# Performance work log

Hardware: AMD Instinct MI355X
Metric: run time of the kernel (lower is better)

Reference implementation:

```python
import jax, jax.numpy as jnp
import numpy as np

_N, _S, _D, _E0 = 30000, 16, 64, 100000


def _build_topology():
    """Windowed subgraphs: root i owns nodes i..i+S-1. Local random edges."""
    N, S, E0 = _N, _S, _E0
    R = N - S + 1                      # number of roots
    rng = np.random.default_rng(0)
    rootid = np.repeat(np.arange(R), S).astype(np.int32)          # [M] tuple -> root i
    nodeid = (rootid + np.tile(np.arange(S), R)).astype(np.int32)  # [M] tuple -> node j
    diag_tuple = (np.arange(R, dtype=np.int64) * S).astype(np.int32)  # tuple index of (i,i)
    # local edges u -> v = u+delta, 1 <= delta < S, so some subgraphs contain both endpoints
    u = rng.integers(0, N - S, E0)
    delta = rng.integers(1, S, E0)
    v = u + delta
    # roots i whose subgraph contains both u and v: max(v-S+1,0) <= i <= u
    lo = np.maximum(v - S + 1, 0)
    cnt = u - lo + 1
    total = int(cnt.sum())
    base = np.repeat(np.cumsum(cnt) - cnt, cnt)
    roots = np.repeat(lo, cnt) + (np.arange(total) - base)
    u_r = np.repeat(u, cnt)
    v_r = np.repeat(v, cnt)
    t_u = roots * S + (u_r - roots)    # tuple index of (i,u)
    t_v = roots * S + (v_r - roots)    # tuple index of (i,v)
    # undirected edge -> both message directions at tuple level
    msg_tgt = np.concatenate([t_u, t_v]).astype(np.int32)
    msg_src = np.concatenate([t_v, t_u]).astype(np.int32)
    return rootid, nodeid, diag_tuple, msg_tgt, msg_src, R


def setup_inputs() -> dict:
    rootid, nodeid, diag_tuple, msg_tgt, msg_src, R = _build_topology()
    M, D = R * _S, _D
    key = jax.random.key(0)
    kx, k0, k1 = jax.random.split(key, 3)
    X = jax.random.normal(kx, (M, D), jnp.float32)
    W0 = jax.random.normal(k0, (D, D), jnp.float32) / np.sqrt(D)
    b0 = jnp.zeros((D,), jnp.float32)
    W1 = jax.random.normal(k1, (3 * D, D), jnp.float32) / np.sqrt(3 * D)
    b1 = jnp.zeros((D,), jnp.float32)
    return {
        "X": X, "W0": W0, "b0": b0, "W1": W1, "b1": b1,
        "rootid": jnp.asarray(rootid), "nodeid": jnp.asarray(nodeid),
        "diag_tuple": jnp.asarray(diag_tuple),
        "msg_tgt": jnp.asarray(msg_tgt), "msg_src": jnp.asarray(msg_src),
        "N": _N,
    }


def reference(X, W0, b0, W1, b1, rootid, nodeid, diag_tuple, msg_tgt, msg_src, N):
    M = X.shape[0]
    R = diag_tuple.shape[0]
    # lin0 (MLP numlayer=1, tailact): tuplewise Linear + ReLU
    H = jax.nn.relu(X @ W0 + b0)                                    # [M, D]
    # 2D message passing on subgraphs: X'_{ij} = sum_{k in N(j)} H_{ik}
    Xmp = jax.ops.segment_sum(H[msg_src], msg_tgt, num_segments=M)  # [M, D]
    ones = jnp.ones((M, 1), X.dtype)
    # diag X_{ii} -> broadcast over subgraph (unpool4subg)
    X1 = Xmp[diag_tuple][rootid]                                    # [M, D]
    # pool over subgraph members j (mean), broadcast back per root i
    Psum = jax.ops.segment_sum(Xmp, rootid, num_segments=R)
    Pcnt = jax.ops.segment_sum(ones, rootid, num_segments=R)
    X2 = (Psum / jnp.maximum(Pcnt, 1.0))[rootid]                    # [M, D]
    # cross-subgraph pool over roots i per node j (mean), broadcast back per node j
    Qsum = jax.ops.segment_sum(Xmp, nodeid, num_segments=N)
    Qcnt = jax.ops.segment_sum(ones, nodeid, num_segments=N)
    X3 = (Qsum / jnp.maximum(Qcnt, 1.0))[nodeid]                    # [M, D]
    # catvalue order: [X2, X1, X3], then final MLP (single Linear)
    return jnp.concatenate([X2, X1, X3], axis=-1) @ W1 + b1         # [M, outdim]
```

## Files before the change

kernel.cpp:

```cpp
#include <hip/hip_runtime.h>

#define S 16
#define D 64
#define G 16
#define PROWS 31
#define PSTR 66
#define PREG 2048
#define XSTR 136
#define ZSTR 68

typedef __attribute__((ext_vector_type(8))) short bf16x8;
typedef __attribute__((ext_vector_type(4))) float f32x4;

union BF8 { unsigned u[4]; bf16x8 v; };

__device__ __forceinline__ unsigned pk2bf(float x, float y) {
    unsigned ux = __float_as_uint(x) + 0x8000u;
    unsigned uy = __float_as_uint(y) + 0x8000u;
    return __builtin_amdgcn_perm(uy, ux, 0x07060302);
}
__device__ __forceinline__ bf16x8 pk8(float a, float b, float c, float d,
                                      float e, float f, float g, float h) {
    BF8 t;
    t.u[0] = pk2bf(a, b); t.u[1] = pk2bf(c, d);
    t.u[2] = pk2bf(e, f); t.u[3] = pk2bf(g, h);
    return t.v;
}
__device__ __forceinline__ unsigned short f2bf_rhu(float x) {
    return (unsigned short)((__float_as_uint(x) + 0x8000u) >> 16);
}
__device__ __forceinline__ short f2bf(float f) {
    unsigned u = __float_as_uint(f);
    u += 0x7fffu + ((u >> 16) & 1u);
    return (short)(u >> 16);
}

__global__ void k_counts(const int* __restrict__ msg_tgt, const int* __restrict__ msg_src,
                         unsigned long long* __restrict__ Q, int E2,
                         const float* __restrict__ W0, const float* __restrict__ W1,
                         unsigned short* __restrict__ W0T, unsigned short* __restrict__ WabT,
                         unsigned short* __restrict__ WcT) {
    int idx = blockIdx.x * 256 + threadIdx.x;
    if (idx < 4096) {
        int d = idx >> 6, k = idx & 63;
        W0T[d * 64 + k] = (unsigned short)f2bf(W0[k * 64 + d]);
    } else if (idx < 12288) {
        int o = idx - 4096; int d = o >> 7, e = o & 127;
        WabT[d * 128 + e] = (unsigned short)f2bf(W1[e * 64 + d]);
    } else if (idx < 16384) {
        int o = idx - 12288; int d = o >> 6, e = o & 63;
        WcT[d * 64 + e] = (unsigned short)f2bf(W1[(128 + e) * 64 + d]);
    }
    if (idx >= E2) return;
    int t = msg_tgt[idx];
    if (t & 15) return;
    int delta = msg_src[idx] & 15;
    int u = t >> 4;
    atomicAdd(&Q[2 * u + 1], 1ull << (4 * delta));
    atomicAdd(&Q[2 * (u + delta)], 1ull << (64 - 4 * delta));
}

__global__ __launch_bounds__(256, 4) void k_root(
    const float* __restrict__ X, const float* __restrict__ b0,
    const unsigned short* __restrict__ W0T,
    const unsigned long long* __restrict__ Q,
    const unsigned short* __restrict__ WabT, const float* __restrict__ b1,
    float* __restrict__ Y, float* __restrict__ Qpart, int R)
{
    __shared__ float part[4 * PREG];
    __shared__ unsigned short x2x1[G][XSTR];
    int grp = blockIdx.x;
    int tid = threadIdx.x, lane = tid & 63, w = tid >> 6, m = lane & 15, q = lane >> 4;
    const ulonglong2* Q2 = (const ulonglong2*)Q;

    {
        float4 z = {0.f, 0.f, 0.f, 0.f};
#pragma unroll
        for (int i = 0; i < 8; i++)
            *(float4*)&part[w * PREG + i * 256 + lane * 4] = z;
    }

    bf16x8 bB[8];
    float bv[4];
#pragma unroll
    for (int cg = 0; cg < 4; cg++) {
        const bf16x8* wr = (const bf16x8*)(W0T + (size_t)(cg * 16 + m) * 64);
        bB[cg * 2] = wr[q]; bB[cg * 2 + 1] = wr[4 + q];
        bv[cg] = b0[cg * 16 + m];
    }

    int bp0 = (((2 * q) * 16 + m) & 63) * 4;
    int bp1 = (((2 * q + 1) * 16 + m) & 63) * 4;

    int root0 = grp * G;
    int gmax = R - root0; if (gmax > G) gmax = G;
    const float* Xg = X + (size_t)root0 * S * D;

    float4 xa, xb, xc, xd; ulonglong2 qq;
    if (w < gmax) {
        const float* xr = Xg + ((size_t)w * S + m) * D + q * 8;
        xa = *(const float4*)(xr);
        xb = *(const float4*)(xr + 4);
        xc = *(const float4*)(xr + 32);
        xd = *(const float4*)(xr + 36);
        qq = Q2[(size_t)(root0 + w) + m];
    }

    for (int g = w; g < gmax; g += 4) {
        float4 nxa, nxb, nxc, nxd; ulonglong2 nqq;
        int gn = g + 4;
        bool pf = (gn < gmax);
        if (pf) {
            const float* xr = Xg + ((size_t)gn * S + m) * D + q * 8;
            nxa = *(const float4*)(xr);
            nxb = *(const float4*)(xr + 4);
            nxc = *(const float4*)(xr + 32);
            nxd = *(const float4*)(xr + 36);
            nqq = Q2[(size_t)(root0 + gn) + m];
        }

        bf16x8 a0 = pk8(xa.x, xa.y, xa.z, xa.w, xb.x, xb.y, xb.z, xb.w);
        bf16x8 a1 = pk8(xc.x, xc.y, xc.z, xc.w, xd.x, xd.y, xd.z, xd.w);
        unsigned hp0[4], hp1[4];
#pragma unroll
        for (int cg = 0; cg < 4; cg++) {
            f32x4 c = {bv[cg], bv[cg], bv[cg], bv[cg]};
            c = __builtin_amdgcn_mfma_f32_16x16x32_bf16(a0, bB[cg * 2], c, 0, 0, 0);
            c = __builtin_amdgcn_mfma_f32_16x16x32_bf16(a1, bB[cg * 2 + 1], c, 0, 0, 0);
            hp0[cg] = pk2bf(fmaxf(c[0], 0.f), fmaxf(c[1], 0.f));
            hp1[cg] = pk2bf(fmaxf(c[2], 0.f), fmaxf(c[3], 0.f));
        }

        unsigned long long cw = (qq.y << (4 * m)) | ((qq.x >> (63 - 4 * m)) >> 1);
        unsigned w32 = (q == 0) ? (unsigned)cw : ((q == 1) ? (unsigned)(cw >> 32) : 0u);
        bf16x8 A2 = pk8((float)((w32 >> 0) & 15u),  (float)((w32 >> 4) & 15u),
                        (float)((w32 >> 8) & 15u),  (float)((w32 >> 12) & 15u),
                        (float)((w32 >> 16) & 15u), (float)((w32 >> 20) & 15u),
                        (float)((w32 >> 24) & 15u), (float)((w32 >> 28) & 15u));

        BF8 b2[4];
#pragma unroll
        for (int cg = 0; cg < 4; cg++) {
            b2[cg].u[0] = __builtin_amdgcn_ds_bpermute(bp0, (int)hp0[cg]);
            b2[cg].u[1] = __builtin_amdgcn_ds_bpermute(bp0, (int)hp1[cg]);
            b2[cg].u[2] = __builtin_amdgcn_ds_bpermute(bp1, (int)hp0[cg]);
            b2[cg].u[3] = __builtin_amdgcn_ds_bpermute(bp1, (int)hp1[cg]);
        }

        f32x4 xm[4];
#pragma unroll
        for (int cg = 0; cg < 4; cg++) {
            f32x4 z4 = {0.f, 0.f, 0.f, 0.f};
            xm[cg] = __builtin_amdgcn_mfma_f32_16x16x32_bf16(A2, b2[cg].v, z4, 0, 0, 0);
        }

        float ps[4], x1[4];
#pragma unroll
        for (int cg = 0; cg < 4; cg++)
            ps[cg] = (xm[cg][0] + xm[cg][1]) + (xm[cg][2] + xm[cg][3]);
#pragma unroll
        for (int cg = 0; cg < 4; cg++) ps[cg] += __shfl_xor(ps[cg], 16);
#pragma unroll
        for (int cg = 0; cg < 4; cg++) ps[cg] += __shfl_xor(ps[cg], 32);
#pragma unroll
        for (int cg = 0; cg < 4; cg++) x1[cg] = __shfl(xm[cg][0], m);
        if (q == 0) {
#pragma unroll
            for (int cg = 0; cg < 4; cg++) {
                x2x1[g][cg * 16 + m]      = f2bf_rhu(ps[cg] * (1.f / 16.f));
                x2x1[g][64 + cg * 16 + m] = f2bf_rhu(x1[cg]);
            }
        }

        int rb = g + q * 4;
#pragma unroll
        for (int cg = 0; cg < 4; cg++) {
            float* pw = &part[w * PREG + rb * PSTR + cg * 16 + m];
            pw[0 * PSTR] += xm[cg][0];
            pw[1 * PSTR] += xm[cg][1];
            pw[2 * PSTR] += xm[cg][2];
            pw[3 * PSTR] += xm[cg][3];
        }

        if (pf) { xa = nxa; xb = nxb; xc = nxc; xd = nxd; qq = nqq; }
    }
    __syncthreads();

    {
        float bvy = b1[w * 16 + m];
        f32x4 c = {bvy, bvy, bvy, bvy};
        const bf16x8* brow = (const bf16x8*)(WabT + (size_t)(w * 16 + m) * 128);
#pragma unroll
        for (int kh = 0; kh < 4; kh++) {
            bf16x8 a = *(const bf16x8*)&x2x1[m][kh * 32 + q * 8];
            c = __builtin_amdgcn_mfma_f32_16x16x32_bf16(a, brow[kh * 4 + q], c, 0, 0, 0);
        }
#pragma unroll
        for (int r = 0; r < 4; r++) {
            int row = root0 + q * 4 + r;
            if (row < R) Y[(size_t)row * 64 + w * 16 + m] = c[r];
        }
    }

    float* qp = Qpart + (size_t)grp * (PROWS * 64);
    for (int idx = tid; idx < PROWS * 32; idx += 256) {
        int r = idx >> 5, c2 = (idx & 31) * 2;
        int o = r * PSTR + c2;
        float2 s0 = *(float2*)&part[o];
        float2 s1 = *(float2*)&part[PREG + o];
        float2 s2 = *(float2*)&part[2 * PREG + o];
        float2 s3 = *(float2*)&part[3 * PREG + o];
        float2 v;
        v.x = s0.x + s1.x + s2.x + s3.x;
        v.y = s0.y + s1.y + s2.y + s3.y;
        *(float2*)&qp[r * 64 + c2] = v;
    }
}

__global__ __launch_bounds__(256) void k_linzout(
    const float* __restrict__ Qpart, const unsigned short* __restrict__ WcT,
    const float* __restrict__ Y, float4* __restrict__ out, int R, int N)
{
    __shared__ float zb[16 * ZSTR];
    int tid = threadIdx.x, lane = tid & 63, w = tid >> 6, m = lane & 15, q = lane >> 4;
    int row0 = blockIdx.x * 16;
    int n = row0 + m;
    float inv = 0.f;
    int gLo = 0, gHi = -1;
    if (n < N) {
        int lo = n - (S - 1); if (lo < 0) lo = 0;
        int hi = (n < R - 1) ? n : (R - 1);
        inv = 1.f / (float)(hi - lo + 1);
        gLo = lo >> 4; gHi = hi >> 4;
    }
    f32x4 c = {0.f, 0.f, 0.f, 0.f};
    const bf16x8* brow = (const bf16x8*)(WcT + (size_t)(w * 16 + m) * 64);
#pragma unroll
    for (int kh = 0; kh < 2; kh++) {
        int k0 = kh * 32 + q * 8;
        float4 u = {0.f, 0.f, 0.f, 0.f}, v = {0.f, 0.f, 0.f, 0.f};
        for (int g = gLo; g <= gHi; g++) {
            const float* src = Qpart + ((size_t)g * PROWS + (n - g * 16)) * 64 + k0;
            float4 uu = *(const float4*)src, vv = *(const float4*)(src + 4);
            u.x += uu.x; u.y += uu.y; u.z += uu.z; u.w += uu.w;
            v.x += vv.x; v.y += vv.y; v.z += vv.z; v.w += vv.w;
        }
        bf16x8 a = pk8(u.x * inv, u.y * inv, u.z * inv, u.w * inv,
                       v.x * inv, v.y * inv, v.z * inv, v.w * inv);
        c = __builtin_amdgcn_mfma_f32_16x16x32_bf16(a, brow[kh * 4 + q], c, 0, 0, 0);
    }
#pragma unroll
    for (int r = 0; r < 4; r++)
        zb[(q * 4 + r) * ZSTR + w * 16 + m] = c[r];
    __syncthreads();

    const float4* Y4 = (const float4*)Y;
#pragma unroll 4
    for (int it = 0; it < 16; ++it) {
        int nl = it;
        int nn = row0 + nl;
        if (nn >= N) break;
        int d4 = tid & 15, ii = tid >> 4;
        int lo = nn - (S - 1); if (lo < 0) lo = 0;
        int hi = (nn < R - 1) ? nn : (R - 1);
        int i = lo + ii;
        if (i > hi) continue;
        int t = i * 16 + (nn - i);
        float4 yv = Y4[(size_t)i * 16 + d4];
        float4 zv = *(float4*)&zb[nl * ZSTR + d4 * 4];
        float4 o;
        o.x = yv.x + zv.x; o.y = yv.y + zv.y; o.z = yv.z + zv.z; o.w = yv.w + zv.w;
        out[(size_t)t * 16 + d4] = o;
    }
}

extern "C" void kernel_launch(void* const* d_in, const int* in_sizes, int n_in,
                              void* d_out, int out_size, void* d_ws, size_t ws_size,
                              hipStream_t stream) {
    (void)n_in; (void)out_size; (void)ws_size;
    const float* X  = (const float*)d_in[0];
    const float* W0 = (const float*)d_in[1];
    const float* b0 = (const float*)d_in[2];
    const float* W1 = (const float*)d_in[3];
    const float* b1 = (const float*)d_in[4];
    const int* msg_tgt = (const int*)d_in[8];
    const int* msg_src = (const int*)d_in[9];
    const int M = in_sizes[5];
    const int R = in_sizes[7];
    const int E = in_sizes[8];
    const int N = R + S - 1;

    char* p = (char*)d_ws;
    unsigned long long* Q = (unsigned long long*)p; p += (size_t)N * 16;
    float* Y    = (float*)p;             p += (size_t)R * 64 * 4;
    unsigned short* W0T  = (unsigned short*)p; p += (size_t)4096 * 2;
    unsigned short* WabT = (unsigned short*)p; p += (size_t)8192 * 2;
    unsigned short* WcT  = (unsigned short*)p; p += (size_t)4096 * 2;

    int NG = (R + G - 1) / G;
    float* Qpart = (float*)d_out;

    hipMemsetAsync(Q, 0, (size_t)N * 16, stream);
    int E2 = E >> 1;
    int CB = (E2 > 16384 ? E2 : 16384);
    k_counts<<<(CB + 255) / 256, 256, 0, stream>>>(msg_tgt, msg_src, Q, E2,
                                                   W0, W1, W0T, WabT, WcT);
    k_root<<<NG, 256, 0, stream>>>(X, b0, W0T, Q, WabT, b1, Y, Qpart, R);
    int NB = (N + 15) / 16;
    k_linzout<<<NB, 256, 0, stream>>>(Qpart, WcT, Y, (float4*)d_out, R, N);
    (void)M;
}
```

Baseline: 275.7 us.

## Compute transposed message MFMA for vectorized partial-sum accumulation and interleave X2/X1

Adds a second MFMA with swapped operands so each lane holds four consecutive columns of the message result. The per-wave shared-memory partial sums can then be read and written as float4 instead of scalar read-modify-writes, with the row stride padded to 68 for alignment. X2 and X1 are packed together into one 32-bit store per column, and the W1 rows are permuted at conversion time to match the interleaved order. The untransposed MFMA result supplies X1 directly, which removes a shuffle. The cost is four extra MFMAs per group and a larger shared-memory footprint.

```diff
diff --git a/kernel.cpp b/kernel.cpp
--- a/kernel.cpp
+++ b/kernel.cpp
@@ -4,8 +4,8 @@
 #define D 64
 #define G 16
 #define PROWS 31
-#define PSTR 66
-#define PREG 2048
+#define PSTR 68
+#define PREG 2176
 #define XSTR 136
 #define ZSTR 68
 
@@ -25,9 +25,6 @@
     t.u[0] = pk2bf(a, b); t.u[1] = pk2bf(c, d);
     t.u[2] = pk2bf(e, f); t.u[3] = pk2bf(g, h);
     return t.v;
-}
-__device__ __forceinline__ unsigned short f2bf_rhu(float x) {
-    return (unsigned short)((__float_as_uint(x) + 0x8000u) >> 16);
 }
 __device__ __forceinline__ short f2bf(float f) {
     unsigned u = __float_as_uint(f);
@@ -46,7 +43,8 @@
         W0T[d * 64 + k] = (unsigned short)f2bf(W0[k * 64 + d]);
     } else if (idx < 12288) {
         int o = idx - 4096; int d = o >> 7, e = o & 127;
-        WabT[d * 128 + e] = (unsigned short)f2bf(W1[e * 64 + d]);
+        int knew = (e < 64) ? (2 * e) : (2 * (e - 64) + 1);
+        WabT[d * 128 + knew] = (unsigned short)f2bf(W1[e * 64 + d]);
     } else if (idx < 16384) {
         int o = idx - 12288; int d = o >> 6, e = o & 63;
         WcT[d * 64 + e] = (unsigned short)f2bf(W1[(128 + e) * 64 + d]);
@@ -78,6 +76,8 @@
 #pragma unroll
         for (int i = 0; i < 8; i++)
             *(float4*)&part[w * PREG + i * 256 + lane * 4] = z;
+        float2 z2 = {0.f, 0.f};
+        *(float2*)&part[w * PREG + 2048 + lane * 2] = z2;
     }
 
     bf16x8 bB[8];
@@ -107,6 +107,11 @@
     }
 
     for (int g = w; g < gmax; g += 4) {
+        float* pbase = &part[w * PREG + (g + m) * PSTR + 4 * q];
+        float4 pr[4];
+#pragma unroll
+        for (int cg = 0; cg < 4; cg++) pr[cg] = *(float4*)&pbase[cg * 16];
+
         float4 nxa, nxb, nxc, nxd; ulonglong2 nqq;
         int gn = g + 4;
         bool pf = (gn < gmax);
@@ -147,39 +152,37 @@
             b2[cg].u[3] = __builtin_amdgcn_ds_bpermute(bp1, (int)hp1[cg]);
         }
 
-        f32x4 xm[4];
+        f32x4 xmt[4];
 #pragma unroll
         for (int cg = 0; cg < 4; cg++) {
             f32x4 z4 = {0.f, 0.f, 0.f, 0.f};
-            xm[cg] = __builtin_amdgcn_mfma_f32_16x16x32_bf16(A2, b2[cg].v, z4, 0, 0, 0);
+            xmt[cg] = __builtin_amdgcn_mfma_f32_16x16x32_bf16(b2[cg].v, A2, z4, 0, 0, 0);
         }
 
         float ps[4], x1[4];
 #pragma unroll
-        for (int cg = 0; cg < 4; cg++)
-            ps[cg] = (xm[cg][0] + xm[cg][1]) + (xm[cg][2] + xm[cg][3]);
+        for (int cg = 0; cg < 4; cg++) {
+            f32x4 z4 = {0.f, 0.f, 0.f, 0.f};
+            f32x4 xu = __builtin_amdgcn_mfma_f32_16x16x32_bf16(A2, b2[cg].v, z4, 0, 0, 0);
+            ps[cg] = (xu[0] + xu[1]) + (xu[2] + xu[3]);
+            x1[cg] = xu[0];
+        }
 #pragma unroll
         for (int cg = 0; cg < 4; cg++) ps[cg] += __shfl_xor(ps[cg], 16);
 #pragma unroll
         for (int cg = 0; cg < 4; cg++) ps[cg] += __shfl_xor(ps[cg], 32);
-#pragma unroll
-        for (int cg = 0; cg < 4; cg++) x1[cg] = __shfl(xm[cg][0], m);
         if (q == 0) {
 #pragma unroll
-            for (int cg = 0; cg < 4; cg++) {
-                x2x1[g][cg * 16 + m]      = f2bf_rhu(ps[cg] * (1.f / 16.f));
-                x2x1[g][64 + cg * 16 + m] = f2bf_rhu(x1[cg]);
-            }
-        }
-
-        int rb = g + q * 4;
-#pragma unroll
-        for (int cg = 0; cg < 4; cg++) {
-            float* pw = &part[w * PREG + rb * PSTR + cg * 16 + m];
-            pw[0 * PSTR] += xm[cg][0];
-            pw[1 * PSTR] += xm[cg][1];
-            pw[2 * PSTR] += xm[cg][2];
-            pw[3 * PSTR] += xm[cg][3];
+            for (int cg = 0; cg < 4; cg++)
+                *(unsigned*)&x2x1[g][2 * (cg * 16 + m)] =
+                    pk2bf(ps[cg] * (1.f / 16.f), x1[cg]);
+        }
+
+#pragma unroll
+        for (int cg = 0; cg < 4; cg++) {
+            pr[cg][0] += xmt[cg][0]; pr[cg][1] += xmt[cg][1];
+            pr[cg][2] += xmt[cg][2]; pr[cg][3] += xmt[cg][3];
+            *(float4*)&pbase[cg * 16] = pr[cg];
         }
 
         if (pf) { xa = nxa; xb = nxb; xc = nxc; xd = nxd; qq = nqq; }
```

Result: slower. 283.3 us (+2.7%).
